# Kernel optimization log

Measured on AMD Instinct MI355X. Metric: run time of the kernel, lower is better.

Reference implementation:

```python
import jax, jax.numpy as jnp
import numpy as np

NEG = -1e30  # log-space 'zero' that keeps gradients finite (vs -inf)


def setup_inputs() -> dict:
    key = jax.random.key(0)
    k1, k2, k3, k4 = jax.random.split(key, 4)
    B, T, V, S = 32, 2048, 128, 256
    predictions = jax.random.normal(k1, (B, T, V), dtype=jnp.float32)
    # input lengths in [T//2, T]; target lengths in [S//4, S]; labels in [1, V) (0 is blank)
    prediction_lengths = jax.random.randint(k2, (B,), T // 2, T + 1, dtype=jnp.int32)
    ground_truths = jax.random.randint(k3, (B, S), 1, V, dtype=jnp.int32)
    ground_truth_lengths = jax.random.randint(k4, (B,), S // 4, S + 1, dtype=jnp.int32)
    return {
        "predictions": predictions,
        "prediction_lengths": prediction_lengths,
        "ground_truths": ground_truths,
        "ground_truth_lengths": ground_truth_lengths,
    }


def _ctc_loss(log_probs, targets, input_lengths, target_lengths, blank=0):
    # log_probs: [T, B, V]; targets: [B, S]
    T, B, V = log_probs.shape
    S = targets.shape[1]
    L = 2 * S + 1  # extended label sequence: blank, l1, blank, l2, ..., blank
    ext = jnp.full((B, L), blank, dtype=targets.dtype).at[:, 1::2].set(targets)
    # skip transition s-2 -> s allowed iff ext[s] != blank and ext[s] != ext[s-2]
    skip = jnp.concatenate(
        [jnp.zeros((B, 2), dtype=bool), (ext[:, 2:] != blank) & (ext[:, 2:] != ext[:, :-2])],
        axis=1,
    )
    # gather per-extended-label log-probs: [T, B, L]
    lp_ext = jnp.take_along_axis(log_probs, jnp.broadcast_to(ext[None], (T, B, L)), axis=2)

    alpha0 = (
        jnp.full((B, L), NEG, dtype=log_probs.dtype)
        .at[:, 0].set(lp_ext[0, :, 0])
        .at[:, 1].set(lp_ext[0, :, 1])
    )

    def step(alpha, lp_t):
        a1 = alpha
        a2 = jnp.pad(alpha[:, :-1], ((0, 0), (1, 0)), constant_values=NEG)
        a3 = jnp.where(skip, jnp.pad(alpha[:, :-2], ((0, 0), (2, 0)), constant_values=NEG), NEG)
        m = jnp.maximum(jnp.maximum(a1, a2), a3)
        new = m + jnp.log(jnp.exp(a1 - m) + jnp.exp(a2 - m) + jnp.exp(a3 - m)) + lp_t
        return new, new

    _, alphas = jax.lax.scan(step, alpha0, lp_ext[1:])
    alphas = jnp.concatenate([alpha0[None], alphas], axis=0)  # [T, B, L]

    bidx = jnp.arange(B)
    alpha_final = alphas[input_lengths - 1, bidx]  # [B, L] at each sequence's last frame
    last = 2 * target_lengths  # index of final blank; last-1 is final label
    loss = -jnp.logaddexp(alpha_final[bidx, last], alpha_final[bidx, last - 1])
    loss = jnp.where(loss < 1e10, loss, 0.0)  # zero_infinity=True
    # torch reduction='mean': per-sample loss / target_length, then batch mean
    return (loss / target_lengths.astype(loss.dtype)).mean()


def reference(predictions, prediction_lengths, ground_truths, ground_truth_lengths):
    # module: transpose to [T, B, V], log_softmax over vocab, then CTC loss
    log_probs = jax.nn.log_softmax(jnp.transpose(predictions, (1, 0, 2)), axis=2)
    return _ctc_loss(log_probs, ground_truths, prediction_lengths, ground_truth_lengths, blank=0)
```

## Files before the change

kernel.cpp:

```cpp
#include <hip/hip_runtime.h>
#include <math.h>

constexpr int V = 128;

__device__ __forceinline__ double dpp_shr1_f64(double x) {
    int lo = __builtin_amdgcn_update_dpp(0, __double2loint(x), 0x138, 0xf, 0xf, false);
    int hi = __builtin_amdgcn_update_dpp(0, __double2hiint(x), 0x138, 0xf, 0xf, false);
    return __hiloint2double(hi, lo);
}
__device__ __forceinline__ double dpp_shl1_f64(double x) {
    int lo = __builtin_amdgcn_update_dpp(0, __double2loint(x), 0x130, 0xf, 0xf, false);
    int hi = __builtin_amdgcn_update_dpp(0, __double2hiint(x), 0x130, 0xf, 0xf, false);
    return __hiloint2double(hi, lo);
}

__global__ __launch_bounds__(256) void ctc_prelude(
    const float* __restrict__ pred, const int* __restrict__ gt,
    const int* __restrict__ gt_len, const int* __restrict__ pred_len,
    float* __restrict__ g, float* __restrict__ z, float* __restrict__ x0a,
    int T, int S)
{
    int wid  = blockIdx.x * 4 + (threadIdx.x >> 6);
    int lane = threadIdx.x & 63;
    int w4   = threadIdx.x >> 6;
    int b    = wid / T;
    int t    = wid - b * T;
    if (t >= pred_len[b]) return;
    __shared__ float rows[4][V];

    const float2* p = (const float2*)pred + (size_t)wid * 64;
    float2 v = p[lane];
    rows[w4][2 * lane]     = v.x;
    rows[w4][2 * lane + 1] = v.y;
    float x0 = __shfl(v.x, 0, 64);
    float s = __expf(v.x) + __expf(v.y);
    #pragma unroll
    for (int off = 32; off >= 1; off >>= 1) s += __shfl_xor(s, off, 64);
    if (lane == 0) { z[wid] = __logf(s); x0a[wid] = v.x; }

    int4 la = *(const int4*)(gt + b * S + 4 * lane);
    int tl = gt_len[b];
    float4 o;
    o.x = (4 * lane + 0 < tl) ? __expf(rows[w4][la.x] - x0) : 0.f;
    o.y = (4 * lane + 1 < tl) ? __expf(rows[w4][la.y] - x0) : 0.f;
    o.z = (4 * lane + 2 < tl) ? __expf(rows[w4][la.z] - x0) : 0.f;
    o.w = (4 * lane + 3 < tl) ? __expf(rows[w4][la.w] - x0) : 0.f;
    *(float4*)(g + (size_t)wid * 256 + 4 * lane) = o;
}

__global__ __launch_bounds__(64) void ctc_scan_bi(
    const float* __restrict__ g,
    const int*   __restrict__ pred_len,
    const int*   __restrict__ gt,
    const int*   __restrict__ gt_len,
    const float* __restrict__ z,
    const float* __restrict__ x0a,
    double*      __restrict__ fwdv,
    double*      __restrict__ bwdv,
    int*         __restrict__ Kf,
    int*         __restrict__ Kb,
    int* done, int* gdone, float* lossb,
    float* __restrict__ out,
    int T, int S, int B)
{
    const int blk  = blockIdx.x;
    const int b    = blk >> 1;
    const int dir  = blk & 1;
    const int lane = threadIdx.x;
    const int len  = pred_len[b];
    const int tl   = gt_len[b];
    const int L    = 2 * tl + 1;
    const int m    = (len + 1) >> 1;

    int4 la = *(const int4*)(gt + b * S + 4 * lane);
    int law_up = __shfl_up(la.w, 1, 64);
    int lax_dn = __shfl_down(la.x, 1, 64);
    const double sk0 = (lane > 0 && la.x != law_up) ? 1.0 : 0.0;
    const double sk1 = (la.y != la.x) ? 1.0 : 0.0;
    const double sk2 = (la.z != la.y) ? 1.0 : 0.0;
    const double sk3 = (la.w != la.z) ? 1.0 : 0.0;
    const double sk4 = (lax_dn != la.w) ? 1.0 : 0.0;

    const char* gb = (const char*)(g + (size_t)b * T * 256) + lane * 16;

    float4 raw[16];
    double u[9];
    int K = 0;

    auto RESCALE = [&]() {
        double mx = u[0];
        #pragma unroll
        for (int j = 1; j < 9; ++j) mx = fmax(mx, u[j]);
        #pragma unroll
        for (int off = 32; off >= 1; off >>= 1)
            mx = fmax(mx, __shfl_xor(mx, off, 64));
        int k = ((__double2hiint(mx) >> 20) & 0x7ff) - 1023;
        #pragma unroll
        for (int j = 0; j < 9; ++j) u[j] = ldexp(u[j], -k);
        K += k;
    };

    if (dir == 0) {
        #pragma unroll
        for (int i = 0; i < 16; ++i)
            raw[i] = *(const float4*)(gb + (size_t)i * 1024);
        #pragma unroll
        for (int j = 0; j < 9; ++j) u[j] = 0.0;
        if (lane == 0) { u[0] = 1.0; u[1] = (double)raw[0].x; }
        raw[0] = *(const float4*)(gb + (size_t)16 * 1024);
        const char* pf = gb + (size_t)17 * 1024;

        auto FSTEP = [&](int i) {
            float4 g4 = raw[i];
            raw[i] = *(const float4*)pf; pf += 1024;
            double um1 = dpp_shr1_f64(u[7]);
            double gx = (double)g4.x, gy = (double)g4.y;
            double gz = (double)g4.z, gw = (double)g4.w;
            u[8] = u[8] + u[7];
            u[7] = (fma(sk3, u[5], u[6]) + u[7]) * gw;
            u[6] = u[6] + u[5];
            u[5] = (fma(sk2, u[3], u[4]) + u[5]) * gz;
            u[4] = u[4] + u[3];
            u[3] = (fma(sk1, u[1], u[2]) + u[3]) * gy;
            u[2] = u[2] + u[1];
            u[1] = (fma(sk0, um1, u[0]) + u[1]) * gx;
            u[0] = u[0] + um1;
        };

        #pragma unroll
        for (int t = 1; t < 16; ++t) FSTEP(t);
        int tb = 16;
        for (; tb + 16 <= m; tb += 16) {
            #pragma unroll
            for (int i = 0; i < 16; ++i) FSTEP(i);
            if (((tb + 16) & 63) == 0) RESCALE();
        }
        #pragma unroll
        for (int i = 0; i < 15; ++i)
            if (tb + i < m) FSTEP(i);
        RESCALE();

        double* outv = fwdv + (size_t)b * 520;
        #pragma unroll
        for (int j = 0; j < 8; ++j) outv[8 * lane + j] = u[j];
        if (lane == 63) outv[512] = u[8];
        if (lane == 0)  Kf[b] = K;
    } else {
        const int nb = len - m;
        #pragma unroll
        for (int i = 0; i < 16; ++i)
            raw[i] = *(const float4*)(gb + (size_t)(len - 1 - i) * 1024);
        #pragma unroll
        for (int j = 0; j < 8; ++j) {
            int s = 8 * lane + j;
            u[j] = (s == 2 * tl || s == 2 * tl - 1) ? 1.0 : 0.0;
        }
        u[8] = (L == 513) ? 1.0 : 0.0;
        const char* pf = gb + (size_t)(len - 17) * 1024;

        auto BSTEP = [&](int i) {
            float4 g4 = raw[i];
            raw[i] = *(const float4*)pf; pf -= 1024;
            double d0 = dpp_shl1_f64(u[0]);
            if (lane == 63) d0 = u[8];
            double p1 = (double)g4.x * u[1], p3 = (double)g4.y * u[3];
            double p5 = (double)g4.z * u[5], p7 = (double)g4.w * u[7];
            double dp = dpp_shl1_f64(p1);
            u[0] = u[0] + p1;
            u[1] = fma(sk1, p3, u[2]) + p1;
            u[2] = u[2] + p3;
            u[3] = fma(sk2, p5, u[4]) + p3;
            u[4] = u[4] + p5;
            u[5] = fma(sk3, p7, u[6]) + p5;
            u[6] = u[6] + p7;
            u[7] = fma(sk4, dp, d0) + p7;
        };

        #pragma unroll
        for (int k = 0; k < 16; ++k) BSTEP(k);
        int kb = 16;
        for (; kb + 16 <= nb; kb += 16) {
            #pragma unroll
            for (int i = 0; i < 16; ++i) BSTEP(i);
            if (((kb + 16) & 63) == 0) RESCALE();
        }
        #pragma unroll
        for (int i = 0; i < 15; ++i)
            if (kb + i < nb) BSTEP(i);
        RESCALE();

        double* outv = bwdv + (size_t)b * 520;
        #pragma unroll
        for (int j = 0; j < 8; ++j) outv[8 * lane + j] = u[j];
        if (lane == 63) outv[512] = u[8];
        if (lane == 0)  Kb[b] = K;
    }

    __threadfence();
    int prev = 0;
    if (lane == 0)
        prev = __hip_atomic_fetch_add(&done[b], 1, __ATOMIC_ACQ_REL,
                                      __HIP_MEMORY_SCOPE_AGENT);
    prev = __shfl(prev, 0, 64);
    if (prev == 0) return;
    __threadfence();

    const double* f = fwdv + (size_t)b * 520;
    const double* w = bwdv + (size_t)b * 520;
    double c = 0.0;
    #pragma unroll
    for (int j = 0; j < 8; ++j)
        c = fma(f[8 * lane + j], w[8 * lane + j], c);
    if (lane == 63) c = fma(f[512], w[512], c);
    #pragma unroll
    for (int off = 32; off >= 1; off >>= 1) c += __shfl_xor(c, off, 64);

    double zs = 0.0;
    for (int t = lane; t < len; t += 64)
        zs += (double)z[b * T + t] - (double)x0a[b * T + t];
    #pragma unroll
    for (int off = 32; off >= 1; off >>= 1) zs += __shfl_xor(zs, off, 64);

    if (lane == 0) {
        double logp = log(c)
                    + (double)(Kf[b] + Kb[b]) * 0.6931471805599453 - zs;
        double loss = -logp;
        if (!(loss < 1e10)) loss = 0.0;
        lossb[b] = (float)(loss / (double)tl);
        __threadfence();
        int pg = __hip_atomic_fetch_add(gdone, 1, __ATOMIC_ACQ_REL,
                                        __HIP_MEMORY_SCOPE_AGENT);
        if (pg == B - 1) {
            __threadfence();
            float ssum = 0.0f;
            for (int i = 0; i < B; ++i) ssum += lossb[i];
            out[0] = ssum / (float)B;
        }
    }
}

constexpr int SPL  = 9;
constexpr int RING = 32;

__global__ void ctc_reduce_kernel(const float* __restrict__ ls,
                                  float* __restrict__ out, int B)
{
    if (blockIdx.x == 0 && threadIdx.x == 0) {
        float s = 0.0f;
        for (int i = 0; i < B; ++i) s += ls[i];
        out[0] = s / (float)B;
    }
}

__global__ __launch_bounds__(256) void softmax_z_kernel(
    const float* __restrict__ pred, float* __restrict__ z, int nrows)
{
    int w    = blockIdx.x * 4 + (threadIdx.x >> 6);
    int lane = threadIdx.x & 63;
    if (w >= nrows) return;
    const float2* p = (const float2*)pred;
    float2 v = p[(size_t)w * 64 + lane];
    float s = __expf(v.x) + __expf(v.y);
    #pragma unroll
    for (int off = 32; off >= 1; off >>= 1) s += __shfl_xor(s, off, 64);
    if (lane == 0) z[w] = __logf(s);
}

__device__ __forceinline__ void ctc_step_fb(
    const float* __restrict__ rowbase, const int* __restrict__ goff,
    const double* __restrict__ skd, double (&u)[SPL], int lane)
{
    float gf[SPL];
    #pragma unroll
    for (int j = 0; j < SPL; ++j)
        gf[j] = *(const float*)((const char*)rowbase + goff[j]);
    double um1 = __shfl_up(u[8], 1, 64);
    double um2 = __shfl_up(u[7], 1, 64);
    if (lane == 0) { um1 = 0.0; um2 = 0.0; }
    #pragma unroll
    for (int jj = 0; jj < SPL; ++jj) {
        int j = SPL - 1 - jj;
        double a2 = (j >= 1) ? u[j - 1] : um1;
        double a3 = (j >= 2) ? u[j - 2] : ((j == 1) ? um1 : um2);
        double t  = fma(skd[j], a3, a2) + u[j];
        u[j] = t * (double)gf[j];
    }
}

__device__ __forceinline__ void ctc_rescale_fb(double (&u)[SPL], int& K)
{
    double m = u[0];
    #pragma unroll
    for (int j = 1; j < SPL; ++j) m = fmax(m, u[j]);
    #pragma unroll
    for (int off = 32; off >= 1; off >>= 1) m = fmax(m, __shfl_xor(m, off, 64));
    if (m > 0.0) {
        int e = (__double2hiint(m) >> 20) & 0x7ff;
        int k = e - 1023;
        #pragma unroll
        for (int j = 0; j < SPL; ++j) u[j] = ldexp(u[j], -k);
        K += k;
    }
}

__global__ __launch_bounds__(64) void ctc_scan_kernel(
    const float* __restrict__ pred, const int* __restrict__ pred_len,
    const int* __restrict__ gt, const int* __restrict__ gt_len,
    const float* __restrict__ z, float* __restrict__ loss_out, int T, int S)
{
    const int b    = blockIdx.x;
    const int lane = threadIdx.x;
    const int len  = pred_len[b];
    const int tl   = gt_len[b];
    const int L    = 2 * tl + 1;

    __shared__ float ring[RING][V];
    __shared__ int   gts[512];

    for (int i = lane; i < S; i += 64) gts[i] = gt[b * S + i];
    __syncthreads();

    int    goff[SPL];
    double skd[SPL];
    #pragma unroll
    for (int j = 0; j < SPL; ++j) {
        int s = SPL * lane + j;
        int e = 0, ep = 0;
        if (s < L && (s & 1)) e = gts[s >> 1];
        if (s >= 2 && s < L && (s & 1)) ep = gts[(s - 2) >> 1];
        goff[j] = e * 4;
        skd[j]  = (s >= 2 && s < L && e != 0 && e != ep) ? 1.0 : 0.0;
    }

    const float2* rowp = (const float2*)(pred + (size_t)b * T * V);
    float2 raw[16];

    #pragma unroll
    for (int i = 0; i < 16; ++i) raw[i] = rowp[(size_t)i * 64 + lane];
    #pragma unroll
    for (int i = 0; i < 16; ++i) {
        float2 w; w.x = __expf(raw[i].x); w.y = __expf(raw[i].y);
        *(float2*)&ring[i][2 * lane] = w;
    }
    #pragma unroll
    for (int i = 0; i < 16; ++i) raw[i] = rowp[(size_t)(16 + i) * 64 + lane];
    #pragma unroll
    for (int i = 0; i < 16; ++i) {
        float2 w; w.x = __expf(raw[i].x); w.y = __expf(raw[i].y);
        *(float2*)&ring[16 + i][2 * lane] = w;
    }
    #pragma unroll
    for (int i = 0; i < 16; ++i) {
        int r = 32 + i; if (r > T - 1) r = T - 1;
        raw[i] = rowp[(size_t)r * 64 + lane];
    }

    double u[SPL];
    #pragma unroll
    for (int j = 0; j < SPL; ++j) {
        int s = SPL * lane + j;
        float w0 = *(const float*)((const char*)&ring[0][0] + goff[j]);
        u[j] = (s < 2) ? (double)w0 : 0.0;
    }
    int K = 0;

    for (int t = 1; t < 16 && t < len; ++t)
        ctc_step_fb(&ring[t & (RING - 1)][0], goff, skd, u, lane);
    ctc_rescale_fb(u, K);

    int tb = 16;
    for (; tb + 16 <= len; tb += 16) {
        #pragma unroll
        for (int i = 0; i < 16; ++i) {
            float2 w; w.x = __expf(raw[i].x); w.y = __expf(raw[i].y);
            *(float2*)&ring[(tb + 16 + i) & (RING - 1)][2 * lane] = w;
        }
        #pragma unroll
        for (int i = 0; i < 16; ++i) {
            int r = tb + 32 + i; if (r > T - 1) r = T - 1;
            raw[i] = rowp[(size_t)r * 64 + lane];
        }
        #pragma unroll
        for (int i = 0; i < 16; ++i)
            ctc_step_fb(&ring[(tb + i) & (RING - 1)][0], goff, skd, u, lane);
        ctc_rescale_fb(u, K);
    }

    for (int t = tb; t < len; ++t)
        ctc_step_fb(&ring[t & (RING - 1)][0], goff, skd, u, lane);

    double contrib = 0.0;
    #pragma unroll
    for (int j = 0; j < SPL; ++j) {
        int s = SPL * lane + j;
        if (s == L - 1 || s == L - 2) contrib += u[j];
    }
    #pragma unroll
    for (int off = 32; off >= 1; off >>= 1)
        contrib += __shfl_xor(contrib, off, 64);

    double zsum = 0.0;
    for (int t = lane; t < len; t += 64) zsum += (double)z[b * T + t];
    #pragma unroll
    for (int off = 32; off >= 1; off >>= 1)
        zsum += __shfl_xor(zsum, off, 64);

    if (lane == 0) {
        double lg    = log(contrib);
        double alpha = lg + (double)K * 0.6931471805599453 - zsum;
        double loss  = -alpha;
        if (!(loss < 1e10)) loss = 0.0;
        loss_out[b] = (float)(loss / (double)tl);
    }
}

extern "C" void kernel_launch(void* const* d_in, const int* in_sizes, int n_in,
                              void* d_out, int out_size, void* d_ws, size_t ws_size,
                              hipStream_t stream) {
    const float* pred = (const float*)d_in[0];
    const int*   plen = (const int*)d_in[1];
    const int*   gts  = (const int*)d_in[2];
    const int*   glen = (const int*)d_in[3];

    const int B = in_sizes[1];
    const int S = in_sizes[2] / B;
    const int T = in_sizes[0] / (B * V);
    const size_t BT = (size_t)B * T;

    float* out = (float*)d_out;
    char*  ws  = (char*)d_ws;

    size_t off_fl  = 0;
    size_t off_z   = 1024;
    size_t off_x0  = off_z   + BT * 4;
    size_t off_fw  = (off_x0 + BT * 4 + 255) & ~(size_t)255;
    size_t off_bw  = off_fw  + (size_t)B * 520 * 8;
    size_t off_kf  = off_bw  + (size_t)B * 520 * 8;
    size_t off_kb  = off_kf  + (size_t)B * 4;
    size_t off_g   = (off_kb + (size_t)B * 4 + 1023) & ~(size_t)1023;
    size_t need    = off_g + BT * 256 * 4;

    bool fast_ok = (ws_size >= need) && (S == 256) && (T % 4 == 0) &&
                   (T >= 96) && (B >= 1) && (B <= 64);

    if (fast_ok) {
        int*    done  = (int*)(ws + off_fl);
        int*    gdone = (int*)(ws + off_fl + 256);
        float*  lossb = (float*)(ws + off_fl + 512);
        float*  zp    = (float*)(ws + off_z);
        float*  x0a   = (float*)(ws + off_x0);
        double* fw    = (double*)(ws + off_fw);
        double* bw    = (double*)(ws + off_bw);
        int*    kf    = (int*)(ws + off_kf);
        int*    kb    = (int*)(ws + off_kb);
        float*  g     = (float*)(ws + off_g);

        hipMemsetAsync(ws + off_fl, 0, 512, stream);
        ctc_prelude<<<B * T / 4, 256, 0, stream>>>(pred, gts, glen, plen,
                                                   g, zp, x0a, T, S);
        ctc_scan_bi<<<2 * B, 64, 0, stream>>>(g, plen, gts, glen, zp, x0a,
                                              fw, bw, kf, kb,
                                              done, gdone, lossb, out, T, S, B);
    } else {
        float* zbuf = (float*)ws;
        float* lb   = zbuf + BT;
        int nrows = B * T;
        softmax_z_kernel<<<(nrows + 3) / 4, 256, 0, stream>>>(pred, zbuf, nrows);
        ctc_scan_kernel<<<B, 64, 0, stream>>>(pred, plen, gts, glen, zbuf, lb, T, S);
        ctc_reduce_kernel<<<1, 64, 0, stream>>>(lb, out, B);
    }
}
```

Before: 174.9 us.

## Deepen scan prefetch ring, fold x0 into z, and drop memset launch

Doubles the register prefetch ring in the bidirectional CTC scan from 16 to 32 frames, so more global-load latency is hidden per step, and sets launch bounds for one block per CU. The prelude now stores z minus x0 in a single array, which removes the x0a buffer and its reads, and it zeroes the completion flags itself, so the separate hipMemsetAsync launch is gone. The final z reduction is unrolled eight-wide. The larger ring raises register pressure and the minimum T, and there is an extra rescale after the warm-up steps plus a clamp on negative loss.

```diff
diff --git a/kernel.cpp b/kernel.cpp
--- a/kernel.cpp
+++ b/kernel.cpp
@@ -17,9 +17,11 @@
 __global__ __launch_bounds__(256) void ctc_prelude(
     const float* __restrict__ pred, const int* __restrict__ gt,
     const int* __restrict__ gt_len, const int* __restrict__ pred_len,
-    float* __restrict__ g, float* __restrict__ z, float* __restrict__ x0a,
+    float* __restrict__ g, float* __restrict__ z, int* __restrict__ flags,
     int T, int S)
 {
+    if (blockIdx.x == 0 && threadIdx.x < 65) flags[threadIdx.x] = 0;
+
     int wid  = blockIdx.x * 4 + (threadIdx.x >> 6);
     int lane = threadIdx.x & 63;
     int w4   = threadIdx.x >> 6;
@@ -36,7 +38,7 @@
     float s = __expf(v.x) + __expf(v.y);
     #pragma unroll
     for (int off = 32; off >= 1; off >>= 1) s += __shfl_xor(s, off, 64);
-    if (lane == 0) { z[wid] = __logf(s); x0a[wid] = v.x; }
+    if (lane == 0) z[wid] = __logf(s) - v.x;
 
     int4 la = *(const int4*)(gt + b * S + 4 * lane);
     int tl = gt_len[b];
@@ -48,13 +50,12 @@
     *(float4*)(g + (size_t)wid * 256 + 4 * lane) = o;
 }
 
-__global__ __launch_bounds__(64) void ctc_scan_bi(
+__global__ __launch_bounds__(64, 1) void ctc_scan_bi(
     const float* __restrict__ g,
     const int*   __restrict__ pred_len,
     const int*   __restrict__ gt,
     const int*   __restrict__ gt_len,
     const float* __restrict__ z,
-    const float* __restrict__ x0a,
     double*      __restrict__ fwdv,
     double*      __restrict__ bwdv,
     int*         __restrict__ Kf,
@@ -83,7 +84,7 @@
 
     const char* gb = (const char*)(g + (size_t)b * T * 256) + lane * 16;
 
-    float4 raw[16];
+    float4 raw[32];
     double u[9];
     int K = 0;
 
@@ -102,13 +103,13 @@
 
     if (dir == 0) {
         #pragma unroll
-        for (int i = 0; i < 16; ++i)
+        for (int i = 0; i < 32; ++i)
             raw[i] = *(const float4*)(gb + (size_t)i * 1024);
         #pragma unroll
         for (int j = 0; j < 9; ++j) u[j] = 0.0;
         if (lane == 0) { u[0] = 1.0; u[1] = (double)raw[0].x; }
-        raw[0] = *(const float4*)(gb + (size_t)16 * 1024);
-        const char* pf = gb + (size_t)17 * 1024;
+        raw[0] = *(const float4*)(gb + (size_t)32 * 1024);
+        const char* pf = gb + (size_t)33 * 1024;
 
         auto FSTEP = [&](int i) {
             float4 g4 = raw[i];
@@ -128,15 +129,16 @@
         };
 
         #pragma unroll
-        for (int t = 1; t < 16; ++t) FSTEP(t);
-        int tb = 16;
-        for (; tb + 16 <= m; tb += 16) {
+        for (int t = 1; t < 32; ++t) FSTEP(t);
+        RESCALE();
+        int tb = 32;
+        for (; tb + 32 <= m; tb += 32) {
             #pragma unroll
-            for (int i = 0; i < 16; ++i) FSTEP(i);
-            if (((tb + 16) & 63) == 0) RESCALE();
-        }
-        #pragma unroll
-        for (int i = 0; i < 15; ++i)
+            for (int i = 0; i < 32; ++i) FSTEP(i);
+            if (((tb + 32) & 63) == 0) RESCALE();
+        }
+        #pragma unroll
+        for (int i = 0; i < 31; ++i)
             if (tb + i < m) FSTEP(i);
         RESCALE();
 
@@ -148,15 +150,15 @@
     } else {
         const int nb = len - m;
         #pragma unroll
-        for (int i = 0; i < 16; ++i)
+        for (int i = 0; i < 32; ++i)
             raw[i] = *(const float4*)(gb + (size_t)(len - 1 - i) * 1024);
         #pragma unroll
         for (int j = 0; j < 8; ++j) {
             int s = 8 * lane + j;
             u[j] = (s == 2 * tl || s == 2 * tl - 1) ? 1.0 : 0.0;
         }
-        u[8] = (L == 513) ? 1.0 : 0.0;
-        const char* pf = gb + (size_t)(len - 17) * 1024;
+        u[8] = (lane == 63 && L == 513) ? 1.0 : 0.0;
+        const char* pf = gb + (size_t)(len - 33) * 1024;
 
         auto BSTEP = [&](int i) {
             float4 g4 = raw[i];
@@ -177,15 +179,16 @@
         };
 
         #pragma unroll
-        for (int k = 0; k < 16; ++k) BSTEP(k);
-        int kb = 16;
-        for (; kb + 16 <= nb; kb += 16) {
+        for (int k = 0; k < 32; ++k) BSTEP(k);
+        RESCALE();
+        int kb = 32;
+        for (; kb + 32 <= nb; kb += 32) {
             #pragma unroll
-            for (int i = 0; i < 16; ++i) BSTEP(i);
-            if (((kb + 16) & 63) == 0) RESCALE();
-        }
-        #pragma unroll
-        for (int i = 0; i < 15; ++i)
+            for (int i = 0; i < 32; ++i) BSTEP(i);
+            if (((kb + 32) & 63) == 0) RESCALE();
+        }
+        #pragma unroll
+        for (int i = 0; i < 31; ++i)
             if (kb + i < nb) BSTEP(i);
         RESCALE();
 
@@ -216,8 +219,16 @@
     for (int off = 32; off >= 1; off >>= 1) c += __shfl_xor(c, off, 64);
 
     double zs = 0.0;
-    for (int t = lane; t < len; t += 64)
-        zs += (double)z[b * T + t] - (double)x0a[b * T + t];
+    const float* zb = z + b * T;
+    int t = lane;
+    for (; t + 448 < len; t += 512) {
+        float a0 = zb[t],       a1 = zb[t + 64],  a2 = zb[t + 128];
+        float a3 = zb[t + 192], a4 = zb[t + 256], a5 = zb[t + 320];
+        float a6 = zb[t + 384], a7 = zb[t + 448];
+        zs += (((double)a0 + a1) + ((double)a2 + a3))
+            + (((double)a4 + a5) + ((double)a6 + a7));
+    }
+    for (; t < len; t += 64) zs += (double)zb[t];
     #pragma unroll
     for (int off = 32; off >= 1; off >>= 1) zs += __shfl_xor(zs, off, 64);
 
@@ -226,6 +237,7 @@
                     + (double)(Kf[b] + Kb[b]) * 0.6931471805599453 - zs;
         double loss = -logp;
         if (!(loss < 1e10)) loss = 0.0;
+        if (loss < 0.0)     loss = 0.0;
         lossb[b] = (float)(loss / (double)tl);
         __threadfence();
         int pg = __hip_atomic_fetch_add(gdone, 1, __ATOMIC_ACQ_REL,
@@ -432,8 +444,7 @@
 
     size_t off_fl  = 0;
     size_t off_z   = 1024;
-    size_t off_x0  = off_z   + BT * 4;
-    size_t off_fw  = (off_x0 + BT * 4 + 255) & ~(size_t)255;
+    size_t off_fw  = (off_z + BT * 4 + 255) & ~(size_t)255;
     size_t off_bw  = off_fw  + (size_t)B * 520 * 8;
     size_t off_kf  = off_bw  + (size_t)B * 520 * 8;
     size_t off_kb  = off_kf  + (size_t)B * 4;
@@ -441,24 +452,23 @@
     size_t need    = off_g + BT * 256 * 4;
 
     bool fast_ok = (ws_size >= need) && (S == 256) && (T % 4 == 0) &&
-                   (T >= 96) && (B >= 1) && (B <= 64);
+                   (T >= 128) && (B >= 1) && (B <= 64);
 
     if (fast_ok) {
-        int*    done  = (int*)(ws + off_fl);
-        int*    gdone = (int*)(ws + off_fl + 256);
+        int*    flags = (int*)(ws + off_fl);
+        int*    done  = flags;
+        int*    gdone = flags + 64;
         float*  lossb = (float*)(ws + off_fl + 512);
         float*  zp    = (float*)(ws + off_z);
-        float*  x0a   = (float*)(ws + off_x0);
         double* fw    = (double*)(ws + off_fw);
         double* bw    = (double*)(ws + off_bw);
         int*    kf    = (int*)(ws + off_kf);
         int*    kb    = (int*)(ws + off_kb);
         float*  g     = (float*)(ws + off_g);
 
-        hipMemsetAsync(ws + off_fl, 0, 512, stream);
         ctc_prelude<<<B * T / 4, 256, 0, stream>>>(pred, gts, glen, plen,
-                                                   g, zp, x0a, T, S);
-        ctc_scan_bi<<<2 * B, 64, 0, stream>>>(g, plen, gts, glen, zp, x0a,
+                                                   g, zp, flags, T, S);
+        ctc_scan_bi<<<2 * B, 64, 0, stream>>>(g, plen, gts, glen, zp,
                                               fw, bw, kf, kb,
                                               done, gdone, lossb, out, T, S, B);
     } else {
```

New measurement: 167.5 us. 4.3% less time.
